# Kernel optimization log

Measured on AMD Instinct MI355X. Metric: run time of the kernel, lower is better.

## Reference

```python
import jax, jax.numpy as jnp
import numpy as np

N, B, DIN, H, D, E = 20000, 2, 128, 4, 64, 320000
NEG_SLOPE = 0.2


def _leaky(x):
    return jnp.where(x >= 0, x, NEG_SLOPE * x)


def setup_inputs() -> dict:
    key = jax.random.key(0)
    k1, k2, k3, k4, k5, k6 = jax.random.split(key, 6)
    feat = jax.random.normal(k1, (N, B, DIN), dtype=jnp.float32)
    # fc weight, xavier-ish scale; stored as (Din, H*D) so projection is feat @ W
    W = jax.random.normal(k2, (DIN, H * D), dtype=jnp.float32) * (1.0 / np.sqrt(DIN))
    attn_l = jax.random.normal(k3, (H, D), dtype=jnp.float32) * 0.1
    attn_r = jax.random.normal(k4, (H, D), dtype=jnp.float32) * 0.1
    src = jax.random.randint(k5, (E,), 0, N, dtype=jnp.int32)
    dst = jax.random.randint(k6, (E,), 0, N, dtype=jnp.int32)
    return {"feat": feat, "W": W, "attn_l": attn_l, "attn_r": attn_r, "src": src, "dst": dst}


def reference(feat, W, attn_l, attn_r, src, dst):
    # feat: (N,B,Din) -> projected features (N,B,H,D)
    ft = (feat @ W).reshape(N, B, H, D)
    # per-node attention logits (N,B,H)
    el = jnp.einsum('nbhd,hd->nbh', ft, attn_l)
    er = jnp.einsum('nbhd,hd->nbh', ft, attn_r)
    # edge logits: u_add_v then LeakyReLU, shape (E,B,H)
    e = _leaky(el[src] + er[dst])
    # edge softmax normalized per destination node (numerically stable)
    emax = jax.ops.segment_max(e, dst, num_segments=N)
    emax = jnp.where(jnp.isfinite(emax), emax, 0.0)  # nodes with no in-edges
    ex = jnp.exp(e - emax[dst])
    denom = jax.ops.segment_sum(ex, dst, num_segments=N)
    a = ex / denom[dst]                               # (E,B,H); denom>0 for every edge's dst
    # u_mul_e messages and sum-aggregation by dst
    m = ft[src] * a[..., None]                        # (E,B,H,D)
    rst = jax.ops.segment_sum(m, dst, num_segments=N)  # (N,B,H,D)
    # module sets self.activation = leaky_relu unconditionally
    return _leaky(rst)
```

## Files before the change

### kernel.cpp

```cpp
#include <hip/hip_runtime.h>
#include <hip/hip_bf16.h>
#include <math.h>


typedef unsigned short ushort;
typedef __attribute__((ext_vector_type(8))) unsigned short ushort8;
typedef __attribute__((ext_vector_type(8))) short short8v;
typedef __attribute__((ext_vector_type(4))) float f32x4;

constexpr int DIN = 128;
constexpr int B   = 2;
constexpr int H   = 4;
constexpr int D   = 64;
constexpr int HD  = H * D;
constexpr int BHD = B * HD;
constexpr int NCOL = 272;
constexpr int PREP_ELEMS  = NCOL * DIN;
constexpr int PREP_BLOCKS = (PREP_ELEMS + 255) / 256;
constexpr int SXS = 72;

__device__ __forceinline__ float leaky(float x) { return x >= 0.f ? x : 0.2f * x; }

__device__ __forceinline__ ushort f2bf(float f) {
    return __builtin_bit_cast(ushort, __float2bfloat16(f));
}
__device__ __forceinline__ float bf2f(ushort v) {
    return __uint_as_float(((unsigned int)v) << 16);
}

__global__ __launch_bounds__(256) void hist_prep_kernel(
    const int* __restrict__ dst, int* __restrict__ deg, int E,
    const float* __restrict__ W, const float* __restrict__ attn_l,
    const float* __restrict__ attn_r, ushort* __restrict__ WT, int histBlocks)
{
    const int t = threadIdx.x;
    const int b = blockIdx.x;
    if (b < histBlocks) {
        int e4 = (b * 256 + t) * 4;
        if (e4 + 3 < E) {
            int4 dd = *(const int4*)(dst + e4);
            atomicAdd(&deg[dd.x], 1); atomicAdd(&deg[dd.y], 1);
            atomicAdd(&deg[dd.z], 1); atomicAdd(&deg[dd.w], 1);
        } else {
            for (int e = e4; e < E; ++e) atomicAdd(&deg[dst[e]], 1);
        }
        return;
    }
    int id = (b - histBlocks) * 256 + t;
    if (id >= PREP_ELEMS) return;
    int c = id >> 7, k = id & 127;
    float v;
    if (c < 256) {
        v = W[k * HD + c];
    } else if (c < 264) {
        int j = c - 256, h = j & 3;
        const float* av = (j < 4 ? attn_l : attn_r) + h * D;
        const float* wp = W + k * HD + h * D;
        float s = 0.f;
        for (int d = 0; d < D; ++d) s = fmaf(wp[d], av[d], s);
        v = s;
    } else {
        v = 0.f;
    }
    WT[c * DIN + k] = f2bf(v);
}

__global__ __launch_bounds__(256) void scan_kernel(
    const int* __restrict__ deg, int* __restrict__ offs,
    int* __restrict__ cursor, int n)
{
    __shared__ int wcarry[4];
    const int t = threadIdx.x;
    const int lane = t & 63;
    const int wid = t >> 6;
    int carry = 0;
    const int nstripes = (n + 1023) >> 10;
    for (int s = 0; s < nstripes; ++s) {
        const int base = (s << 10) + t * 4;
        int4 d = make_int4(0, 0, 0, 0);
        if (base + 3 < n) {
            d = *(const int4*)(deg + base);
        } else {
            if (base     < n) d.x = deg[base];
            if (base + 1 < n) d.y = deg[base + 1];
            if (base + 2 < n) d.z = deg[base + 2];
        }
        const int sum4 = (d.x + d.y) + (d.z + d.w);
        int inc = sum4;
#pragma unroll
        for (int o = 1; o < 64; o <<= 1) {
            int v = __shfl_up(inc, o, 64);
            if (lane >= o) inc += v;
        }
        if (lane == 63) wcarry[wid] = inc;
        __syncthreads();
        int wpre = carry;
#pragma unroll
        for (int k = 0; k < 4; ++k) if (k < wid) wpre += wcarry[k];
        const int e0 = wpre + inc - sum4;
        int4 ov;
        ov.x = e0; ov.y = e0 + d.x; ov.z = ov.y + d.y; ov.w = ov.z + d.z;
        if (base + 3 < n) {
            *(int4*)(offs + base) = ov;
            *(int4*)(cursor + base) = ov;
        } else {
            if (base     < n) { offs[base]     = ov.x; cursor[base]     = ov.x; }
            if (base + 1 < n) { offs[base + 1] = ov.y; cursor[base + 1] = ov.y; }
            if (base + 2 < n) { offs[base + 2] = ov.z; cursor[base + 2] = ov.z; }
        }
        carry += (wcarry[0] + wcarry[1]) + (wcarry[2] + wcarry[3]);
        __syncthreads();
    }
    if (t == 0) offs[n] = carry;
}

__global__ __launch_bounds__(256) void proj_scatter_kernel(
    const float* __restrict__ feat, const ushort* __restrict__ WT,
    ushort* __restrict__ ftb, float* __restrict__ el, float* __restrict__ er,
    const int* __restrict__ dst, const int* __restrict__ src,
    int* __restrict__ cursor, int* __restrict__ esrc, int E,
    int nTiles, int PB)
{
    if ((int)blockIdx.x >= PB) {
        int e4 = (((int)blockIdx.x - PB) * 256 + (int)threadIdx.x) * 4;
        if (e4 + 3 < E) {
            int4 dd = *(const int4*)(dst + e4);
            int4 ss = *(const int4*)(src + e4);
            int p0 = atomicAdd(&cursor[dd.x], 1); esrc[p0] = ss.x;
            int p1 = atomicAdd(&cursor[dd.y], 1); esrc[p1] = ss.y;
            int p2 = atomicAdd(&cursor[dd.z], 1); esrc[p2] = ss.z;
            int p3 = atomicAdd(&cursor[dd.w], 1); esrc[p3] = ss.w;
        } else {
            for (int e = e4; e < E; ++e) {
                int pos = atomicAdd(&cursor[dst[e]], 1);
                esrc[pos] = src[e];
            }
        }
        return;
    }

    __shared__ ushort sxp[4][2][16][SXS];
    const int t = threadIdx.x;
    const int w = t >> 6;
    const int lane = t & 63;
    const int lr = lane & 15;
    const int lk = lane >> 4;

    short8v bfrag[4][4];
#pragma unroll
    for (int ct = 0; ct < 4; ++ct) {
        const int col = w * 64 + ct * 16 + lr;
#pragma unroll
        for (int ks = 0; ks < 4; ++ks)
            bfrag[ct][ks] = *(const short8v*)&WT[col * DIN + ks * 32 + lk * 8];
    }
    short8v efrag[4];
#pragma unroll
    for (int ks = 0; ks < 4; ++ks)
        efrag[ks] = *(const short8v*)&WT[(256 + lr) * DIN + ks * 32 + lk * 8];

    const int rrow = lane >> 2;
    const int seg  = lane & 3;

    for (int tile = blockIdx.x; tile < nTiles; tile += PB) {
        const int row0 = tile * 64;

        auto loadA = [&](int rt, short8v aout[4]) {
            const float* fp = feat + (size_t)(row0 + rt * 16 + lr) * DIN + lk * 8;
#pragma unroll
            for (int ks = 0; ks < 4; ++ks) {
                f32x4 x0 = *(const f32x4*)(fp + ks * 32);
                f32x4 x1 = *(const f32x4*)(fp + ks * 32 + 4);
                short8v v;
                v[0] = (short)f2bf(x0[0]); v[1] = (short)f2bf(x0[1]);
                v[2] = (short)f2bf(x0[2]); v[3] = (short)f2bf(x0[3]);
                v[4] = (short)f2bf(x1[0]); v[5] = (short)f2bf(x1[1]);
                v[6] = (short)f2bf(x1[2]); v[7] = (short)f2bf(x1[3]);
                aout[ks] = v;
            }
        };

        short8v aP[4], aN[4];
        loadA(0, aP);

#pragma unroll
        for (int rt = 0; rt < 4; ++rt) {
            if (rt < 3) loadA(rt + 1, aN);

            f32x4 acc[4] = {{0.f,0.f,0.f,0.f},{0.f,0.f,0.f,0.f},{0.f,0.f,0.f,0.f},{0.f,0.f,0.f,0.f}};
#pragma unroll
            for (int ct = 0; ct < 4; ++ct)
#pragma unroll
                for (int ks = 0; ks < 4; ++ks)
                    acc[ct] = __builtin_amdgcn_mfma_f32_16x16x32_bf16(aP[ks], bfrag[ct][ks], acc[ct], 0, 0, 0);

            ushort (* __restrict__ sw)[SXS] = sxp[w][rt & 1];
#pragma unroll
            for (int ct = 0; ct < 4; ++ct)
#pragma unroll
                for (int r = 0; r < 4; ++r)
                    sw[lk * 4 + r][ct * 16 + lr] = f2bf(acc[ct][r]);
            __builtin_amdgcn_wave_barrier();
            ushort8 o0 = *(const ushort8*)&sw[rrow][seg * 16];
            ushort8 o1 = *(const ushort8*)&sw[rrow][seg * 16 + 8];
            ushort* gp = ftb + (size_t)(row0 + rt * 16 + rrow) * HD + w * 64 + seg * 16;
            *(ushort8*)gp = o0;
            *(ushort8*)(gp + 8) = o1;

            if (rt == w) {
                f32x4 acce = {0.f, 0.f, 0.f, 0.f};
#pragma unroll
                for (int ks = 0; ks < 4; ++ks)
                    acce = __builtin_amdgcn_mfma_f32_16x16x32_bf16(aP[ks], efrag[ks], acce, 0, 0, 0);
#pragma unroll
                for (int r = 0; r < 4; ++r) {
                    const int row = row0 + rt * 16 + lk * 4 + r;
                    if (lr < 4)       el[row * 4 + lr]       = acce[r];
                    else if (lr < 8)  er[row * 4 + (lr - 4)] = acce[r];
                }
            }

#pragma unroll
            for (int ks = 0; ks < 4; ++ks) aP[ks] = aN[ks];
        }
    }
}

__global__ __launch_bounds__(256) void agg_kernel(
    const ushort* __restrict__ ftb, const float* __restrict__ el,
    const float* __restrict__ er, const int* __restrict__ offs,
    const int* __restrict__ esrc, float* __restrict__ out, int N)
{
    const int t = threadIdx.x;
    const int n = blockIdx.x * 4 + (t >> 6);
    if (n >= N) return;
    const int lane = t & 63;
    const int bh = lane >> 3;
    const int beg = offs[n];
    const int end = offs[n + 1];

    const float erd = er[n * 8 + bh];
    const ushort8* __restrict__ ftv = (const ushort8*)ftb;

    float acc[8];
#pragma unroll
    for (int j = 0; j < 8; ++j) acc[j] = 0.f;
    float dsum = 0.f;

    int i = beg;
    if (end - beg >= 8) {
        int sA[4]; ushort8 vA[4]; float xA[4];
#pragma unroll
        for (int u = 0; u < 4; ++u) sA[u] = esrc[i + u];
#pragma unroll
        for (int u = 0; u < 4; ++u) vA[u] = ftv[(unsigned)sA[u] * 64 + lane];
#pragma unroll
        for (int u = 0; u < 4; ++u) xA[u] = el[sA[u] * 8 + bh];

        for (; i + 7 < end; i += 4) {
            int sB[4]; ushort8 vB[4]; float xB[4];
#pragma unroll
            for (int u = 0; u < 4; ++u) sB[u] = esrc[i + 4 + u];
#pragma unroll
            for (int u = 0; u < 4; ++u) vB[u] = ftv[(unsigned)sB[u] * 64 + lane];
#pragma unroll
            for (int u = 0; u < 4; ++u) xB[u] = el[sB[u] * 8 + bh];

            float w[4];
#pragma unroll
            for (int u = 0; u < 4; ++u) { w[u] = __expf(leaky(xA[u] + erd)); }
            dsum += (w[0] + w[1]) + (w[2] + w[3]);
#pragma unroll
            for (int j = 0; j < 8; ++j) {
                float a = acc[j];
#pragma unroll
                for (int u = 0; u < 4; ++u) a = fmaf(w[u], bf2f(vA[u][j]), a);
                acc[j] = a;
            }
#pragma unroll
            for (int u = 0; u < 4; ++u) { sA[u] = sB[u]; vA[u] = vB[u]; xA[u] = xB[u]; }
        }
        float w[4];
#pragma unroll
        for (int u = 0; u < 4; ++u) { w[u] = __expf(leaky(xA[u] + erd)); }
        dsum += (w[0] + w[1]) + (w[2] + w[3]);
#pragma unroll
        for (int j = 0; j < 8; ++j) {
            float a = acc[j];
#pragma unroll
            for (int u = 0; u < 4; ++u) a = fmaf(w[u], bf2f(vA[u][j]), a);
            acc[j] = a;
        }
        i += 4;
    }
    for (; i < end; ++i) {
        int s0 = esrc[i];
        ushort8 v0 = ftv[(unsigned)s0 * 64 + lane];
        float w0 = __expf(leaky(el[s0 * 8 + bh] + erd));
        dsum += w0;
#pragma unroll
        for (int j = 0; j < 8; ++j) acc[j] = fmaf(w0, bf2f(v0[j]), acc[j]);
    }

    const float sc = (end > beg) ? (1.f / dsum) : 0.f;
    float4 o0, o1;
    o0.x = leaky(acc[0] * sc); o0.y = leaky(acc[1] * sc);
    o0.z = leaky(acc[2] * sc); o0.w = leaky(acc[3] * sc);
    o1.x = leaky(acc[4] * sc); o1.y = leaky(acc[5] * sc);
    o1.z = leaky(acc[6] * sc); o1.w = leaky(acc[7] * sc);
    float* op = out + (size_t)n * BHD + lane * 8;
    *(float4*)op = o0;
    *(float4*)(op + 4) = o1;
}

extern "C" void kernel_launch(void* const* d_in, const int* in_sizes, int n_in,
                              void* d_out, int out_size, void* d_ws, size_t ws_size,
                              hipStream_t stream)
{
    const float* feat   = (const float*)d_in[0];
    const float* W      = (const float*)d_in[1];
    const float* attn_l = (const float*)d_in[2];
    const float* attn_r = (const float*)d_in[3];
    const int*   src    = (const int*)d_in[4];
    const int*   dst    = (const int*)d_in[5];
    float* out = (float*)d_out;

    const int N = in_sizes[0] / (B * DIN);
    const int E = in_sizes[4];
    const int R = N * B;
    const int nTiles = R / 64;
    const int projBlocks = (nTiles + 1) / 2;
    const int histBlocks = (E / 4 + 255) / 256;
    const int edgeBlocks = histBlocks;

    auto align_up = [](size_t x) { return (x + 255) & ~(size_t)255; };
    size_t off = 0;
    char* base = (char*)d_ws;
    ushort* ftb = (ushort*)(base + off); off += align_up((size_t)R * HD * sizeof(ushort));
    float* el   = (float*)(base + off); off += align_up((size_t)R * H * sizeof(float));
    float* er   = (float*)(base + off); off += align_up((size_t)R * H * sizeof(float));
    ushort* WT  = (ushort*)(base + off); off += align_up((size_t)NCOL * DIN * sizeof(ushort));
    int* deg    = (int*)(base + off); off += align_up((size_t)N * sizeof(int));
    int* offs   = (int*)(base + off); off += align_up((size_t)(N + 1) * sizeof(int));
    int* cursor = (int*)(base + off); off += align_up((size_t)N * sizeof(int));
    int* esrc   = (int*)(base + off); off += align_up((size_t)E * sizeof(int));
    (void)ws_size; (void)n_in; (void)out_size;

    hipMemsetAsync(deg, 0, (size_t)N * sizeof(int), stream);

    hist_prep_kernel<<<histBlocks + PREP_BLOCKS, 256, 0, stream>>>(
        dst, deg, E, W, attn_l, attn_r, WT, histBlocks);
    scan_kernel<<<1, 256, 0, stream>>>(deg, offs, cursor, N);
    proj_scatter_kernel<<<projBlocks + edgeBlocks, 256, 0, stream>>>(
        feat, WT, ftb, el, er, dst, src, cursor, esrc, E, nTiles, projBlocks);
    agg_kernel<<<(N + 3) / 4, 256, 0, stream>>>(ftb, el, er, offs, esrc, out, N);
}
```

Before: 116.3 us.

## Sort aggregation nodes by in-degree and give each projection tile its own block

The single-block scan kernel now also counting-sorts nodes into descending in-degree buckets, producing a permutation that the aggregation kernel uses so heavy nodes are scheduled first and waves within a block have similar work. The projection kernel drops its grid-stride loop and launches one block per 64-row tile, so there are twice as many projection blocks. The sort adds serial work to the already single-block scan kernel, with shared-memory atomics contending on a few buckets, and the permuted node order loses sequential output locality in aggregation.

```diff
diff --git a/kernel.cpp b/kernel.cpp
--- a/kernel.cpp
+++ b/kernel.cpp
@@ -67,9 +67,10 @@
 
 __global__ __launch_bounds__(256) void scan_kernel(
     const int* __restrict__ deg, int* __restrict__ offs,
-    int* __restrict__ cursor, int n)
+    int* __restrict__ cursor, int* __restrict__ nperm, int n)
 {
     __shared__ int wcarry[4];
+    __shared__ int bbase[64];
     const int t = threadIdx.x;
     const int lane = t & 63;
     const int wid = t >> 6;
@@ -112,6 +113,21 @@
         __syncthreads();
     }
     if (t == 0) offs[n] = carry;
+
+    if (t < 64) bbase[t] = 0;
+    __syncthreads();
+    for (int i = t; i < n; i += 256)
+        atomicAdd(&bbase[min(deg[i], 63)], 1);
+    __syncthreads();
+    if (t == 0) {
+        int run = 0;
+        for (int b = 63; b >= 0; --b) { int c = bbase[b]; bbase[b] = run; run += c; }
+    }
+    __syncthreads();
+    for (int i = t; i < n; i += 256) {
+        int pos = atomicAdd(&bbase[min(deg[i], 63)], 1);
+        nperm[pos] = i;
+    }
 }
 
 __global__ __launch_bounds__(256) void proj_scatter_kernel(
@@ -119,10 +135,10 @@
     ushort* __restrict__ ftb, float* __restrict__ el, float* __restrict__ er,
     const int* __restrict__ dst, const int* __restrict__ src,
     int* __restrict__ cursor, int* __restrict__ esrc, int E,
-    int nTiles, int PB)
-{
-    if ((int)blockIdx.x >= PB) {
-        int e4 = (((int)blockIdx.x - PB) * 256 + (int)threadIdx.x) * 4;
+    int nTiles)
+{
+    if ((int)blockIdx.x >= nTiles) {
+        int e4 = (((int)blockIdx.x - nTiles) * 256 + (int)threadIdx.x) * 4;
         if (e4 + 3 < E) {
             int4 dd = *(const int4*)(dst + e4);
             int4 ss = *(const int4*)(src + e4);
@@ -161,79 +177,78 @@
 
     const int rrow = lane >> 2;
     const int seg  = lane & 3;
-
-    for (int tile = blockIdx.x; tile < nTiles; tile += PB) {
-        const int row0 = tile * 64;
-
-        auto loadA = [&](int rt, short8v aout[4]) {
-            const float* fp = feat + (size_t)(row0 + rt * 16 + lr) * DIN + lk * 8;
-#pragma unroll
-            for (int ks = 0; ks < 4; ++ks) {
-                f32x4 x0 = *(const f32x4*)(fp + ks * 32);
-                f32x4 x1 = *(const f32x4*)(fp + ks * 32 + 4);
-                short8v v;
-                v[0] = (short)f2bf(x0[0]); v[1] = (short)f2bf(x0[1]);
-                v[2] = (short)f2bf(x0[2]); v[3] = (short)f2bf(x0[3]);
-                v[4] = (short)f2bf(x1[0]); v[5] = (short)f2bf(x1[1]);
-                v[6] = (short)f2bf(x1[2]); v[7] = (short)f2bf(x1[3]);
-                aout[ks] = v;
+    const int row0 = blockIdx.x * 64;
+
+    auto loadA = [&](int rt, short8v aout[4]) {
+        const float* fp = feat + (size_t)(row0 + rt * 16 + lr) * DIN + lk * 8;
+#pragma unroll
+        for (int ks = 0; ks < 4; ++ks) {
+            f32x4 x0 = *(const f32x4*)(fp + ks * 32);
+            f32x4 x1 = *(const f32x4*)(fp + ks * 32 + 4);
+            short8v v;
+            v[0] = (short)f2bf(x0[0]); v[1] = (short)f2bf(x0[1]);
+            v[2] = (short)f2bf(x0[2]); v[3] = (short)f2bf(x0[3]);
+            v[4] = (short)f2bf(x1[0]); v[5] = (short)f2bf(x1[1]);
+            v[6] = (short)f2bf(x1[2]); v[7] = (short)f2bf(x1[3]);
+            aout[ks] = v;
+        }
+    };
+
+    short8v aP[4], aN[4];
+    loadA(0, aP);
+
+#pragma unroll
+    for (int rt = 0; rt < 4; ++rt) {
+        if (rt < 3) loadA(rt + 1, aN);
+
+        f32x4 acc[4] = {{0.f,0.f,0.f,0.f},{0.f,0.f,0.f,0.f},{0.f,0.f,0.f,0.f},{0.f,0.f,0.f,0.f}};
+#pragma unroll
+        for (int ct = 0; ct < 4; ++ct)
+#pragma unroll
+            for (int ks = 0; ks < 4; ++ks)
+                acc[ct] = __builtin_amdgcn_mfma_f32_16x16x32_bf16(aP[ks], bfrag[ct][ks], acc[ct], 0, 0, 0);
+
+        ushort (* __restrict__ sw)[SXS] = sxp[w][rt & 1];
+#pragma unroll
+        for (int ct = 0; ct < 4; ++ct)
+#pragma unroll
+            for (int r = 0; r < 4; ++r)
+                sw[lk * 4 + r][ct * 16 + lr] = f2bf(acc[ct][r]);
+        __builtin_amdgcn_wave_barrier();
+        ushort8 o0 = *(const ushort8*)&sw[rrow][seg * 16];
+        ushort8 o1 = *(const ushort8*)&sw[rrow][seg * 16 + 8];
+        ushort* gp = ftb + (size_t)(row0 + rt * 16 + rrow) * HD + w * 64 + seg * 16;
+        *(ushort8*)gp = o0;
+        *(ushort8*)(gp + 8) = o1;
+
+        if (rt == w) {
+            f32x4 acce = {0.f, 0.f, 0.f, 0.f};
+#pragma unroll
+            for (int ks = 0; ks < 4; ++ks)
+                acce = __builtin_amdgcn_mfma_f32_16x16x32_bf16(aP[ks], efrag[ks], acce, 0, 0, 0);
+#pragma unroll
+            for (int r = 0; r < 4; ++r) {
+                const int row = row0 + rt * 16 + lk * 4 + r;
+                if (lr < 4)       el[row * 4 + lr]       = acce[r];
+                else if (lr < 8)  er[row * 4 + (lr - 4)] = acce[r];
             }
-        };
-
-        short8v aP[4], aN[4];
-        loadA(0, aP);
-
-#pragma unroll
-        for (int rt = 0; rt < 4; ++rt) {
-            if (rt < 3) loadA(rt + 1, aN);
-
-            f32x4 acc[4] = {{0.f,0.f,0.f,0.f},{0.f,0.f,0.f,0.f},{0.f,0.f,0.f,0.f},{0.f,0.f,0.f,0.f}};
-#pragma unroll
-            for (int ct = 0; ct < 4; ++ct)
-#pragma unroll
-                for (int ks = 0; ks < 4; ++ks)
-                    acc[ct] = __builtin_amdgcn_mfma_f32_16x16x32_bf16(aP[ks], bfrag[ct][ks], acc[ct], 0, 0, 0);
-
-            ushort (* __restrict__ sw)[SXS] = sxp[w][rt & 1];
-#pragma unroll
-            for (int ct = 0; ct < 4; ++ct)
-#pragma unroll
-                for (int r = 0; r < 4; ++r)
-                    sw[lk * 4 + r][ct * 16 + lr] = f2bf(acc[ct][r]);
-            __builtin_amdgcn_wave_barrier();
-            ushort8 o0 = *(const ushort8*)&sw[rrow][seg * 16];
-            ushort8 o1 = *(const ushort8*)&sw[rrow][seg * 16 + 8];
-            ushort* gp = ftb + (size_t)(row0 + rt * 16 + rrow) * HD + w * 64 + seg * 16;
-            *(ushort8*)gp = o0;
-            *(ushort8*)(gp + 8) = o1;
-
-            if (rt == w) {
-                f32x4 acce = {0.f, 0.f, 0.f, 0.f};
-#pragma unroll
-                for (int ks = 0; ks < 4; ++ks)
-                    acce = __builtin_amdgcn_mfma_f32_16x16x32_bf16(aP[ks], efrag[ks], acce, 0, 0, 0);
-#pragma unroll
-                for (int r = 0; r < 4; ++r) {
-                    const int row = row0 + rt * 16 + lk * 4 + r;
-                    if (lr < 4)       el[row * 4 + lr]       = acce[r];
-                    else if (lr < 8)  er[row * 4 + (lr - 4)] = acce[r];
-                }
-            }
-
-#pragma unroll
-            for (int ks = 0; ks < 4; ++ks) aP[ks] = aN[ks];
-        }
+        }
+
+#pragma unroll
+        for (int ks = 0; ks < 4; ++ks) aP[ks] = aN[ks];
     }
 }
 
 __global__ __launch_bounds__(256) void agg_kernel(
     const ushort* __restrict__ ftb, const float* __restrict__ el,
     const float* __restrict__ er, const int* __restrict__ offs,
-    const int* __restrict__ esrc, float* __restrict__ out, int N)
+    const int* __restrict__ esrc, const int* __restrict__ nperm,
+    float* __restrict__ out, int N)
 {
     const int t = threadIdx.x;
-    const int n = blockIdx.x * 4 + (t >> 6);
-    if (n >= N) return;
+    const int slot = blockIdx.x * 4 + (t >> 6);
+    if (slot >= N) return;
+    const int n = nperm[slot];
     const int lane = t & 63;
     const int bh = lane >> 3;
     const int beg = offs[n];
@@ -329,7 +344,6 @@
     const int E = in_sizes[4];
     const int R = N * B;
     const int nTiles = R / 64;
-    const int projBlocks = (nTiles + 1) / 2;
     const int histBlocks = (E / 4 + 255) / 256;
     const int edgeBlocks = histBlocks;
 
@@ -343,6 +357,7 @@
     int* deg    = (int*)(base + off); off += align_up((size_t)N * sizeof(int));
     int* offs   = (int*)(base + off); off += align_up((size_t)(N + 1) * sizeof(int));
     int* cursor = (int*)(base + off); off += align_up((size_t)N * sizeof(int));
+    int* nperm  = (int*)(base + off); off += align_up((size_t)N * sizeof(int));
     int* esrc   = (int*)(base + off); off += align_up((size_t)E * sizeof(int));
     (void)ws_size; (void)n_in; (void)out_size;
 
@@ -350,8 +365,8 @@
 
     hist_prep_kernel<<<histBlocks + PREP_BLOCKS, 256, 0, stream>>>(
         dst, deg, E, W, attn_l, attn_r, WT, histBlocks);
-    scan_kernel<<<1, 256, 0, stream>>>(deg, offs, cursor, N);
-    proj_scatter_kernel<<<projBlocks + edgeBlocks, 256, 0, stream>>>(
-        feat, WT, ftb, el, er, dst, src, cursor, esrc, E, nTiles, projBlocks);
-    agg_kernel<<<(N + 3) / 4, 256, 0, stream>>>(ftb, el, er, offs, esrc, out, N);
-}
+    scan_kernel<<<1, 256, 0, stream>>>(deg, offs, cursor, nperm, N);
+    proj_scatter_kernel<<<nTiles + edgeBlocks, 256, 0, stream>>>(
+        feat, WT, ftb, el, er, dst, src, cursor, esrc, E, nTiles);
+    agg_kernel<<<(N + 3) / 4, 256, 0, stream>>>(ftb, el, er, offs, esrc, nperm, out, N);
+}
```

Measured after the change: 148.8 us. 28.0% more time.

## Pre-convert features to bf16 in histogram kernel; one tile per projection block

Applied to the files above, without the earlier changes.

Moves the fp32-to-bf16 conversion of the input features into the first kernel, where it runs alongside the degree histogram, which is followed by the serial single-block scan. The projection kernel then loads bf16 directly and launches one block per 64-row tile instead of looping over two tiles per block. This hides the conversion work behind the scan bubble and halves the bytes the projection kernel reads. In exchange it writes and rereads an extra bf16 copy of the features.

```diff
diff --git a/kernel.cpp b/kernel.cpp
--- a/kernel.cpp
+++ b/kernel.cpp
@@ -28,10 +28,12 @@
     return __uint_as_float(((unsigned int)v) << 16);
 }
 
-__global__ __launch_bounds__(256) void hist_prep_kernel(
+__global__ __launch_bounds__(256) void hist_prep_cvt_kernel(
     const int* __restrict__ dst, int* __restrict__ deg, int E,
     const float* __restrict__ W, const float* __restrict__ attn_l,
-    const float* __restrict__ attn_r, ushort* __restrict__ WT, int histBlocks)
+    const float* __restrict__ attn_r, ushort* __restrict__ WT,
+    const float* __restrict__ feat, ushort* __restrict__ featb, int R,
+    int histBlocks)
 {
     const int t = threadIdx.x;
     const int b = blockIdx.x;
@@ -46,23 +48,35 @@
         }
         return;
     }
-    int id = (b - histBlocks) * 256 + t;
-    if (id >= PREP_ELEMS) return;
-    int c = id >> 7, k = id & 127;
-    float v;
-    if (c < 256) {
-        v = W[k * HD + c];
-    } else if (c < 264) {
-        int j = c - 256, h = j & 3;
-        const float* av = (j < 4 ? attn_l : attn_r) + h * D;
-        const float* wp = W + k * HD + h * D;
-        float s = 0.f;
-        for (int d = 0; d < D; ++d) s = fmaf(wp[d], av[d], s);
-        v = s;
-    } else {
-        v = 0.f;
-    }
-    WT[c * DIN + k] = f2bf(v);
+    if (b < histBlocks + PREP_BLOCKS) {
+        int id = (b - histBlocks) * 256 + t;
+        if (id >= PREP_ELEMS) return;
+        int c = id >> 7, k = id & 127;
+        float v;
+        if (c < 256) {
+            v = W[k * HD + c];
+        } else if (c < 264) {
+            int j = c - 256, h = j & 3;
+            const float* av = (j < 4 ? attn_l : attn_r) + h * D;
+            const float* wp = W + k * HD + h * D;
+            float s = 0.f;
+            for (int d = 0; d < D; ++d) s = fmaf(wp[d], av[d], s);
+            v = s;
+        } else {
+            v = 0.f;
+        }
+        WT[c * DIN + k] = f2bf(v);
+        return;
+    }
+    size_t g8 = ((size_t)(b - histBlocks - PREP_BLOCKS) * 256 + t) * 8;
+    if (g8 + 7 < (size_t)R * DIN) {
+        f32x4 x0 = *(const f32x4*)(feat + g8);
+        f32x4 x1 = *(const f32x4*)(feat + g8 + 4);
+        ushort8 v;
+        v[0] = f2bf(x0[0]); v[1] = f2bf(x0[1]); v[2] = f2bf(x0[2]); v[3] = f2bf(x0[3]);
+        v[4] = f2bf(x1[0]); v[5] = f2bf(x1[1]); v[6] = f2bf(x1[2]); v[7] = f2bf(x1[3]);
+        *(ushort8*)(featb + g8) = v;
+    }
 }
 
 __global__ __launch_bounds__(256) void scan_kernel(
@@ -115,14 +129,14 @@
 }
 
 __global__ __launch_bounds__(256) void proj_scatter_kernel(
-    const float* __restrict__ feat, const ushort* __restrict__ WT,
+    const ushort* __restrict__ featb, const ushort* __restrict__ WT,
     ushort* __restrict__ ftb, float* __restrict__ el, float* __restrict__ er,
     const int* __restrict__ dst, const int* __restrict__ src,
     int* __restrict__ cursor, int* __restrict__ esrc, int E,
-    int nTiles, int PB)
-{
-    if ((int)blockIdx.x >= PB) {
-        int e4 = (((int)blockIdx.x - PB) * 256 + (int)threadIdx.x) * 4;
+    int nTiles)
+{
+    if ((int)blockIdx.x >= nTiles) {
+        int e4 = (((int)blockIdx.x - nTiles) * 256 + (int)threadIdx.x) * 4;
         if (e4 + 3 < E) {
             int4 dd = *(const int4*)(dst + e4);
             int4 ss = *(const int4*)(src + e4);
@@ -161,68 +175,57 @@
 
     const int rrow = lane >> 2;
     const int seg  = lane & 3;
-
-    for (int tile = blockIdx.x; tile < nTiles; tile += PB) {
-        const int row0 = tile * 64;
-
-        auto loadA = [&](int rt, short8v aout[4]) {
-            const float* fp = feat + (size_t)(row0 + rt * 16 + lr) * DIN + lk * 8;
-#pragma unroll
-            for (int ks = 0; ks < 4; ++ks) {
-                f32x4 x0 = *(const f32x4*)(fp + ks * 32);
-                f32x4 x1 = *(const f32x4*)(fp + ks * 32 + 4);
-                short8v v;
-                v[0] = (short)f2bf(x0[0]); v[1] = (short)f2bf(x0[1]);
-                v[2] = (short)f2bf(x0[2]); v[3] = (short)f2bf(x0[3]);
-                v[4] = (short)f2bf(x1[0]); v[5] = (short)f2bf(x1[1]);
-                v[6] = (short)f2bf(x1[2]); v[7] = (short)f2bf(x1[3]);
-                aout[ks] = v;
+    const int row0 = blockIdx.x * 64;
+
+    auto loadA = [&](int rt, short8v aout[4]) {
+        const ushort* fp = featb + (size_t)(row0 + rt * 16 + lr) * DIN + lk * 8;
+#pragma unroll
+        for (int ks = 0; ks < 4; ++ks)
+            aout[ks] = *(const short8v*)(fp + ks * 32);
+    };
+
+    short8v aP[4], aN[4];
+    loadA(0, aP);
+
+#pragma unroll
+    for (int rt = 0; rt < 4; ++rt) {
+        if (rt < 3) loadA(rt + 1, aN);
+
+        f32x4 acc[4] = {{0.f,0.f,0.f,0.f},{0.f,0.f,0.f,0.f},{0.f,0.f,0.f,0.f},{0.f,0.f,0.f,0.f}};
+#pragma unroll
+        for (int ct = 0; ct < 4; ++ct)
+#pragma unroll
+            for (int ks = 0; ks < 4; ++ks)
+                acc[ct] = __builtin_amdgcn_mfma_f32_16x16x32_bf16(aP[ks], bfrag[ct][ks], acc[ct], 0, 0, 0);
+
+        ushort (* __restrict__ sw)[SXS] = sxp[w][rt & 1];
+#pragma unroll
+        for (int ct = 0; ct < 4; ++ct)
+#pragma unroll
+            for (int r = 0; r < 4; ++r)
+                sw[lk * 4 + r][ct * 16 + lr] = f2bf(acc[ct][r]);
+        __builtin_amdgcn_wave_barrier();
+        ushort8 o0 = *(const ushort8*)&sw[rrow][seg * 16];
+        ushort8 o1 = *(const ushort8*)&sw[rrow][seg * 16 + 8];
+        ushort* gp = ftb + (size_t)(row0 + rt * 16 + rrow) * HD + w * 64 + seg * 16;
+        *(ushort8*)gp = o0;
+        *(ushort8*)(gp + 8) = o1;
+
+        if (rt == w) {
+            f32x4 acce = {0.f, 0.f, 0.f, 0.f};
+#pragma unroll
+            for (int ks = 0; ks < 4; ++ks)
+                acce = __builtin_amdgcn_mfma_f32_16x16x32_bf16(aP[ks], efrag[ks], acce, 0, 0, 0);
+#pragma unroll
+            for (int r = 0; r < 4; ++r) {
+                const int row = row0 + rt * 16 + lk * 4 + r;
+                if (lr < 4)       el[row * 4 + lr]       = acce[r];
+                else if (lr < 8)  er[row * 4 + (lr - 4)] = acce[r];
             }
-        };
-
-        short8v aP[4], aN[4];
-        loadA(0, aP);
-
-#pragma unroll
-        for (int rt = 0; rt < 4; ++rt) {
-            if (rt < 3) loadA(rt + 1, aN);
-
-            f32x4 acc[4] = {{0.f,0.f,0.f,0.f},{0.f,0.f,0.f,0.f},{0.f,0.f,0.f,0.f},{0.f,0.f,0.f,0.f}};
-#pragma unroll
-            for (int ct = 0; ct < 4; ++ct)
-#pragma unroll
-                for (int ks = 0; ks < 4; ++ks)
-                    acc[ct] = __builtin_amdgcn_mfma_f32_16x16x32_bf16(aP[ks], bfrag[ct][ks], acc[ct], 0, 0, 0);
-
-            ushort (* __restrict__ sw)[SXS] = sxp[w][rt & 1];
-#pragma unroll
-            for (int ct = 0; ct < 4; ++ct)
-#pragma unroll
-                for (int r = 0; r < 4; ++r)
-                    sw[lk * 4 + r][ct * 16 + lr] = f2bf(acc[ct][r]);
-            __builtin_amdgcn_wave_barrier();
-            ushort8 o0 = *(const ushort8*)&sw[rrow][seg * 16];
-            ushort8 o1 = *(const ushort8*)&sw[rrow][seg * 16 + 8];
-            ushort* gp = ftb + (size_t)(row0 + rt * 16 + rrow) * HD + w * 64 + seg * 16;
-            *(ushort8*)gp = o0;
-            *(ushort8*)(gp + 8) = o1;
-
-            if (rt == w) {
-                f32x4 acce = {0.f, 0.f, 0.f, 0.f};
-#pragma unroll
-                for (int ks = 0; ks < 4; ++ks)
-                    acce = __builtin_amdgcn_mfma_f32_16x16x32_bf16(aP[ks], efrag[ks], acce, 0, 0, 0);
-#pragma unroll
-                for (int r = 0; r < 4; ++r) {
-                    const int row = row0 + rt * 16 + lk * 4 + r;
-                    if (lr < 4)       el[row * 4 + lr]       = acce[r];
-                    else if (lr < 8)  er[row * 4 + (lr - 4)] = acce[r];
-                }
-            }
-
-#pragma unroll
-            for (int ks = 0; ks < 4; ++ks) aP[ks] = aN[ks];
-        }
+        }
+
+#pragma unroll
+        for (int ks = 0; ks < 4; ++ks) aP[ks] = aN[ks];
     }
 }
 
@@ -329,14 +332,15 @@
     const int E = in_sizes[4];
     const int R = N * B;
     const int nTiles = R / 64;
-    const int projBlocks = (nTiles + 1) / 2;
     const int histBlocks = (E / 4 + 255) / 256;
     const int edgeBlocks = histBlocks;
+    const int cvtBlocks  = (R * (DIN / 8) + 255) / 256;
 
     auto align_up = [](size_t x) { return (x + 255) & ~(size_t)255; };
     size_t off = 0;
     char* base = (char*)d_ws;
-    ushort* ftb = (ushort*)(base + off); off += align_up((size_t)R * HD * sizeof(ushort));
+    ushort* ftb   = (ushort*)(base + off); off += align_up((size_t)R * HD * sizeof(ushort));
+    ushort* featb = (ushort*)(base + off); off += align_up((size_t)R * DIN * sizeof(ushort));
     float* el   = (float*)(base + off); off += align_up((size_t)R * H * sizeof(float));
     float* er   = (float*)(base + off); off += align_up((size_t)R * H * sizeof(float));
     ushort* WT  = (ushort*)(base + off); off += align_up((size_t)NCOL * DIN * sizeof(ushort));
@@ -348,10 +352,10 @@
 
     hipMemsetAsync(deg, 0, (size_t)N * sizeof(int), stream);
 
-    hist_prep_kernel<<<histBlocks + PREP_BLOCKS, 256, 0, stream>>>(
-        dst, deg, E, W, attn_l, attn_r, WT, histBlocks);
+    hist_prep_cvt_kernel<<<histBlocks + PREP_BLOCKS + cvtBlocks, 256, 0, stream>>>(
+        dst, deg, E, W, attn_l, attn_r, WT, feat, featb, R, histBlocks);
     scan_kernel<<<1, 256, 0, stream>>>(deg, offs, cursor, N);
-    proj_scatter_kernel<<<projBlocks + edgeBlocks, 256, 0, stream>>>(
-        feat, WT, ftb, el, er, dst, src, cursor, esrc, E, nTiles, projBlocks);
+    proj_scatter_kernel<<<nTiles + edgeBlocks, 256, 0, stream>>>(
+        featb, WT, ftb, el, er, dst, src, cursor, esrc, E, nTiles);
     agg_kernel<<<(N + 3) / 4, 256, 0, stream>>>(ftb, el, er, offs, esrc, out, N);
 }
```

Result: slower. 120.9 us (+4.0%).
